# Performance work log

Measured on AMD Instinct MI355X. Metric: run time of the kernel, lower is better.

Reference implementation:

```python
import jax, jax.numpy as jnp
import numpy as np

D_MODEL = 1024
N_HEADS = 16
D_HEAD = D_MODEL // N_HEADS
GN_EPS = 1e-5


def setup_inputs() -> dict:
    key = jax.random.key(0)
    ks = jax.random.split(key, 5)
    B, T = 2, 2048
    s = 1.0 / np.sqrt(D_MODEL)
    x = jax.random.normal(ks[0], (B, T, D_MODEL), dtype=jnp.float32)
    W_q = jax.random.normal(ks[1], (D_MODEL, D_MODEL), dtype=jnp.float32) * s
    W_k = jax.random.normal(ks[2], (D_MODEL, D_MODEL), dtype=jnp.float32) * s
    W_v = jax.random.normal(ks[3], (D_MODEL, D_MODEL), dtype=jnp.float32) * s
    W_o = jax.random.normal(ks[4], (D_MODEL, D_MODEL), dtype=jnp.float32) * s
    gn_weight = jnp.ones((D_MODEL,), dtype=jnp.float32)
    gn_bias = jnp.zeros((D_MODEL,), dtype=jnp.float32)
    return {"x": x, "W_q": W_q, "W_k": W_k, "W_v": W_v, "W_o": W_o,
            "gn_weight": gn_weight, "gn_bias": gn_bias}


def reference(x, W_q, W_k, W_v, W_o, gn_weight, gn_bias):
    B, T, _ = x.shape
    H, Dh = N_HEADS, D_HEAD
    # Projections (nn.Linear: y = x @ W.T), split heads -> [B, T, H, Dh]
    q = (x @ W_q.T).reshape(B, T, H, Dh)
    k = (x @ W_k.T).reshape(B, T, H, Dh)
    v = (x @ W_v.T).reshape(B, T, H, Dh)

    # Per-head causal decay mask D_h[i, j] = gamma_h^(i-j) for i >= j else 0
    gammas = jnp.asarray([1.0 - 2.0 ** (-5.0 - i) for i in range(H)],
                         dtype=jnp.float32)  # [H]
    idx = jnp.arange(T, dtype=jnp.float32)
    diff = idx[:, None] - idx[None, :]  # [T, T]
    decay = jnp.where(diff >= 0,
                      gammas[:, None, None] ** jnp.maximum(diff, 0.0),
                      0.0)  # [H, T, T]

    scale = jnp.sqrt(jnp.asarray(Dh, dtype=x.dtype))
    qk = jnp.einsum('bthd,bshd->bhts', q, k)          # [B, H, T, T]
    attn = qk * decay[None] / scale
    y = jnp.einsum('bhts,bshd->bthd', attn, v)        # [B, T, H, Dh]

    # GroupNorm(n_heads groups) over channels-last-transposed layout:
    # torch applies it to [B, d_model, T]; each group = one head's Dh channels,
    # normalized over (Dh, T).
    yg = y.transpose(0, 2, 3, 1)                      # [B, H, Dh, T]
    mean = yg.mean(axis=(2, 3), keepdims=True)
    var = yg.var(axis=(2, 3), keepdims=True)
    yn = (yg - mean) / jnp.sqrt(var + GN_EPS)
    yn = yn * gn_weight.reshape(1, H, Dh, 1) + gn_bias.reshape(1, H, Dh, 1)
    y = yn.transpose(0, 3, 1, 2).reshape(B, T, H * Dh)  # [B, T, d_model]
    return y @ W_o.T
```

## Files before the change

kernel.cpp:

```cpp
#include <hip/hip_runtime.h>
#include <math.h>

#define TSEQ 2048
#define NB   2
#define DM   1024
#define NH   16
#define DH   64
#define GN_EPS 1e-5f

typedef short v8s __attribute__((ext_vector_type(8)));
typedef short v4s __attribute__((ext_vector_type(4)));
typedef float v4f __attribute__((ext_vector_type(4)));

__device__ __forceinline__ short f2bf(float f) {
    union { float f; unsigned u; } c; c.f = f;
    unsigned u = c.u;
    unsigned r = (u + 0x7fffu + ((u >> 16) & 1u)) >> 16;
    return (short)r;
}
__device__ __forceinline__ float bf2f(short s) {
    union { unsigned u; float f; } c; c.u = ((unsigned)(unsigned short)s) << 16;
    return c.f;
}

__device__ __forceinline__ unsigned cvtpk_bf16(float lo, float hi) {
    unsigned r;
    asm("v_cvt_pk_bf16_f32 %0, %1, %2" : "=v"(r) : "v"(lo), "v"(hi));
    return r;
}

__device__ __forceinline__ void gl_lds16(const void* g, void* l) {
    __builtin_amdgcn_global_load_lds(
        (const __attribute__((address_space(1))) void*)g,
        (__attribute__((address_space(3))) void*)l, 16, 0, 0);
}

__global__ __launch_bounds__(256) void cast_kernel(
    const float* __restrict__ x,
    const float* __restrict__ Wq, const float* __restrict__ Wk,
    const float* __restrict__ Wv, const float* __restrict__ Wo,
    short* __restrict__ xbf, short* __restrict__ wbf)
{
    const int NX = NB * TSEQ * DM;
    const int NW = DM * DM;
    const int total4 = (NX + 4 * NW) / 4;
    for (int i = blockIdx.x * 256 + threadIdx.x; i < total4;
         i += gridDim.x * 256) {
        int e = i * 4;
        const float* src; short* dst;
        if (e < NX) { src = x + e; dst = xbf + e; }
        else {
            int o = e - NX;
            int w = o >> 20;
            int r = o & (NW - 1);
            src = (w == 0 ? Wq : w == 1 ? Wk : w == 2 ? Wv : Wo) + r;
            dst = wbf + o;
        }
        v4f v = *(const v4f*)src;
        v4s s;
        #pragma unroll
        for (int j = 0; j < 4; ++j) s[j] = f2bf(v[j]);
        *(v4s*)dst = s;
    }
}

__global__ __launch_bounds__(256, 3) void gemm_qkv_mfma(
    const short* __restrict__ xbf, const short* __restrict__ wbf,
    short* __restrict__ Qb, short* __restrict__ Kb,
    short* __restrict__ Kt, short* __restrict__ Vt)
{
    const int z = blockIdx.z;
    const short* __restrict__ Bmat = wbf + (size_t)z * (DM * DM);
    const int n0 = blockIdx.x * 128, m0 = blockIdx.y * 128;
    const int t = threadIdx.x, l = t & 63, w = t >> 6;
    const int wr = (w >> 1) * 64, wc = (w & 1) * 64;
    const int lr = l & 15, g = l >> 4, lg4 = g * 4;

    __shared__ short As[128 * 64];
    __shared__ short Bs[128 * 64];

    v4f acc[4][4];
    #pragma unroll
    for (int i = 0; i < 4; ++i)
        #pragma unroll
        for (int j = 0; j < 4; ++j) acc[i][j] = (v4f){0.f, 0.f, 0.f, 0.f};

    const char* Agp = (const char*)(xbf  + (size_t)m0 * DM);
    const char* Bgp = (const char*)(Bmat + (size_t)n0 * DM);

    int soff[4], sdst[4];
    #pragma unroll
    for (int p = 0; p < 4; ++p) {
        int i = p * 256 + t;
        int row = i >> 3;
        int cp  = (i & 7) * 16;
        soff[p] = row * (DM * 2) + (cp ^ ((row & 7) << 4));
        sdst[p] = (p * 256 + (t & 192)) * 16;
    }
    const int swz = (lr & 7) << 4;

    for (int kt = 0; kt < DM / 64; ++kt) {
        const int kb = kt * 128;
        #pragma unroll
        for (int p = 0; p < 4; ++p) {
            gl_lds16(Agp + (size_t)soff[p] + kb, (char*)As + sdst[p]);
            gl_lds16(Bgp + (size_t)soff[p] + kb, (char*)Bs + sdst[p]);
        }
        asm volatile("s_waitcnt vmcnt(0)" ::: "memory");
        __syncthreads();

        v8s bfr[4][2];
        #pragma unroll
        for (int j = 0; j < 4; ++j) {
            int rowb = wc + j * 16 + lr;
            #pragma unroll
            for (int ks = 0; ks < 2; ++ks)
                bfr[j][ks] = *(const v8s*)((const char*)Bs + rowb * 128
                               + ((ks * 64 + g * 16) ^ swz));
        }
        #pragma unroll
        for (int i = 0; i < 4; ++i) {
            int rowa = wr + i * 16 + lr;
            v8s a0 = *(const v8s*)((const char*)As + rowa * 128 + ((g * 16) ^ swz));
            v8s a1 = *(const v8s*)((const char*)As + rowa * 128 + ((64 + g * 16) ^ swz));
            #pragma unroll
            for (int j = 0; j < 4; ++j) {
                acc[i][j] = __builtin_amdgcn_mfma_f32_16x16x32_bf16(
                    a0, bfr[j][0], acc[i][j], 0, 0, 0);
                acc[i][j] = __builtin_amdgcn_mfma_f32_16x16x32_bf16(
                    a1, bfr[j][1], acc[i][j], 0, 0, 0);
            }
        }
        __syncthreads();
    }

    if (z == 0) {
        float l2gj[4];
        #pragma unroll
        for (int j = 0; j < 4; ++j) {
            int hh = (n0 + wc + j * 16 + lr) >> 6;
            l2gj[j] = log2f(1.0f - exp2f(-5.0f - (float)hh));
        }
        #pragma unroll
        for (int i = 0; i < 4; ++i) {
            int row = m0 + wr + i * 16 + lg4;
            #pragma unroll
            for (int j = 0; j < 4; ++j) {
                int col = n0 + wc + j * 16 + lr;
                #pragma unroll
                for (int r = 0; r < 4; ++r) {
                    int tl = (row + r) & 63;
                    float fac = exp2f(fmaf(l2gj[j], (float)tl, -3.0f));
                    Qb[(size_t)(row + r) * DM + col] = f2bf(acc[i][j][r] * fac);
                }
            }
        }
    } else if (z == 1) {
        float l2gj[4];
        #pragma unroll
        for (int j = 0; j < 4; ++j) {
            int hh = (n0 + wc + j * 16 + lr) >> 6;
            l2gj[j] = -log2f(1.0f - exp2f(-5.0f - (float)hh));
        }
        #pragma unroll
        for (int i = 0; i < 4; ++i) {
            int row  = m0 + wr + i * 16 + lg4;
            int bidx = row >> 11, tb = row & (TSEQ - 1);
            #pragma unroll
            for (int j = 0; j < 4; ++j) {
                int col = n0 + wc + j * 16 + lr;
                v4s pk;
                #pragma unroll
                for (int r = 0; r < 4; ++r) {
                    int tl = (row + r) & 63;
                    float fac = exp2f(l2gj[j] * (float)tl);
                    short bv = f2bf(acc[i][j][r] * fac);
                    Kb[(size_t)(row + r) * DM + col] = bv;
                    pk[r] = bv;
                }
                *(v4s*)(Kt + ((size_t)bidx << 21) + ((size_t)col << 11) + tb) = pk;
            }
        }
    } else {
        #pragma unroll
        for (int i = 0; i < 4; ++i) {
            int row  = m0 + wr + i * 16 + lg4;
            int bidx = row >> 11, tb = row & (TSEQ - 1);
            #pragma unroll
            for (int j = 0; j < 4; ++j) {
                int col = n0 + wc + j * 16 + lr;
                v4s pk;
                #pragma unroll
                for (int r = 0; r < 4; ++r) pk[r] = f2bf(acc[i][j][r]);
                *(v4s*)(Vt + ((size_t)bidx << 21) + ((size_t)col << 11) + tb) = pk;
            }
        }
    }
}

__global__ __launch_bounds__(256, 2) void chunk_kv(
    const short* __restrict__ Kt, const short* __restrict__ Vt,
    short* __restrict__ At)
{
    const int bid = blockIdx.x;
    const int c = bid & 31, bh = bid >> 5;
    const int b = bh >> 4, h = bh & 15;
    const int tid = threadIdx.x, l = tid & 63, w = tid >> 6;
    const int lr = l & 15, g = l >> 4;

    const size_t rowbase = ((size_t)b * DM + h * 64);

    v8s kf[2], vf[4][2];
    {
        const short* kp = Kt + (rowbase + 16 * w + lr) * TSEQ + 64 * c;
        kf[0] = *(const v8s*)(kp + g * 8);
        kf[1] = *(const v8s*)(kp + 32 + g * 8);
    }
    #pragma unroll
    for (int j = 0; j < 4; ++j) {
        const short* vp = Vt + (rowbase + j * 16 + lr) * TSEQ + 64 * c;
        vf[j][0] = *(const v8s*)(vp + g * 8);
        vf[j][1] = *(const v8s*)(vp + 32 + g * 8);
    }

    v4f acc[4];
    #pragma unroll
    for (int j = 0; j < 4; ++j) acc[j] = (v4f){0.f, 0.f, 0.f, 0.f};

    #pragma unroll
    for (int j = 0; j < 4; ++j) {
        acc[j] = __builtin_amdgcn_mfma_f32_16x16x32_bf16(kf[0], vf[j][0], acc[j], 0, 0, 0);
        acc[j] = __builtin_amdgcn_mfma_f32_16x16x32_bf16(kf[1], vf[j][1], acc[j], 0, 0, 0);
    }

    short* Ab = At + (((size_t)bh * 32 + c) << 12);
    #pragma unroll
    for (int j = 0; j < 4; ++j) {
        v4s pk;
        #pragma unroll
        for (int r = 0; r < 4; ++r) pk[r] = f2bf(acc[j][r]);
        *(v4s*)(Ab + (j * 16 + lr) * 64 + 16 * w + g * 4) = pk;
    }
}

__global__ __launch_bounds__(256) void chunk_scan(
    const short* __restrict__ At, short* __restrict__ St)
{
    const int idx = blockIdx.x * 256 + threadIdx.x;
    const int bh = idx >> 12;
    const int h  = bh & 15;
    const float l2g = log2f(1.0f - exp2f(-5.0f - (float)h));
    const float g64 = exp2f(l2g * 64.0f);

    const size_t base = ((size_t)bh << 17) + (idx & 4095);
    float state = 0.0f;
    #pragma unroll
    for (int c = 1; c < 32; ++c) {
        float a = bf2f(At[base + ((size_t)(c - 1) << 12)]);
        state = g64 * (state + a);
        St[base + ((size_t)c << 12)] = f2bf(state);
    }
}

__global__ __launch_bounds__(256, 2) void chunk_out(
    const short* __restrict__ Qb, const short* __restrict__ Kb,
    const short* __restrict__ Vt, const short* __restrict__ St,
    short* __restrict__ Ybf, float* __restrict__ psums)
{
    const int bid = blockIdx.x;
    const int xcd = bid & 7, r8 = bid >> 3;
    const int bh  = xcd * 4 + (r8 >> 5);
    const int c   = r8 & 31;
    const int b = bh >> 4, h = bh & 15;
    const int tid = threadIdx.x, l = tid & 63, w = tid >> 6;
    const int lr = l & 15, g = l >> 4;

    __shared__ short strip[64 * 64];
    __shared__ float tr[64][68];
    __shared__ float red[8];

    const size_t rowQK = ((size_t)(b * TSEQ + 64 * c)) * DM + h * 64;

    v8s qf[4][2];
    #pragma unroll
    for (int j = 0; j < 4; ++j) {
        const short* qp = Qb + rowQK + (size_t)(j * 16 + lr) * DM;
        qf[j][0] = *(const v8s*)(qp + g * 8);
        qf[j][1] = *(const v8s*)(qp + 32 + g * 8);
    }
    v8s kf0, kf1;
    {
        const short* kp = Kb + rowQK + (size_t)(16 * w + lr) * DM;
        kf0 = *(const v8s*)(kp + g * 8);
        kf1 = *(const v8s*)(kp + 32 + g * 8);
    }
    v8s sf0 = {}, sf1 = {};
    if (c > 0) {
        const short* sp = St + (((size_t)bh * 32 + c) << 12) + (16 * w + lr) * 64;
        sf0 = *(const v8s*)(sp + g * 8);
        sf1 = *(const v8s*)(sp + 32 + g * 8);
    }
    v8s vf0, vf1;
    {
        const short* vp = Vt + ((size_t)(b * DM + h * 64) + 16 * w + lr) * TSEQ
                          + 64 * c;
        vf0 = *(const v8s*)(vp + g * 8);
        vf1 = *(const v8s*)(vp + 32 + g * 8);
    }

    v4f s[4];
    #pragma unroll
    for (int j = 0; j < 4; ++j) {
        v4f a = (v4f){0.f, 0.f, 0.f, 0.f};
        a = __builtin_amdgcn_mfma_f32_16x16x32_bf16(kf0, qf[j][0], a, 0, 0, 0);
        a = __builtin_amdgcn_mfma_f32_16x16x32_bf16(kf1, qf[j][1], a, 0, 0, 0);
        s[j] = a;
    }

    v4f y[4];
    #pragma unroll
    for (int j = 0; j < 4; ++j) y[j] = (v4f){0.f, 0.f, 0.f, 0.f};
    if (c > 0) {
        #pragma unroll
        for (int j = 0; j < 4; ++j) {
            y[j] = __builtin_amdgcn_mfma_f32_16x16x32_bf16(sf0, qf[j][0], y[j], 0, 0, 0);
            y[j] = __builtin_amdgcn_mfma_f32_16x16x32_bf16(sf1, qf[j][1], y[j], 0, 0, 0);
        }
    }

    #pragma unroll
    for (int j = 0; j < 4; ++j) {
        v4f vv = s[j];
        #pragma unroll
        for (int r = 0; r < 4; ++r)
            if ((j * 16 + lr) - (16 * w + g * 4 + r) < 0) vv[r] = 0.0f;
        unsigned u0 = cvtpk_bf16(vv[0], vv[1]);
        unsigned u1 = cvtpk_bf16(vv[2], vv[3]);
        int byte = ((j * 16 + lr) * 128 + 32 * w + g * 8) ^ ((lr & 7) << 4);
        *(unsigned long long*)((char*)strip + byte) =
            (unsigned long long)u0 | ((unsigned long long)u1 << 32);
    }
    __syncthreads();

    #pragma unroll
    for (int j = 0; j < 4; ++j) {
        int rb = (j * 16 + lr) * 128;
        int sw = (lr & 7) << 4;
        v8s sB0 = *(const v8s*)((char*)strip + ((rb + g * 16) ^ sw));
        v8s sB1 = *(const v8s*)((char*)strip + ((rb + 64 + g * 16) ^ sw));
        y[j] = __builtin_amdgcn_mfma_f32_16x16x32_bf16(vf0, sB0, y[j], 0, 0, 0);
        y[j] = __builtin_amdgcn_mfma_f32_16x16x32_bf16(vf1, sB1, y[j], 0, 0, 0);
    }

    float lsum = 0.f, lsq = 0.f;
    #pragma unroll
    for (int j = 0; j < 4; ++j)
        #pragma unroll
        for (int r = 0; r < 4; ++r) {
            float vy = y[j][r];
            lsum += vy; lsq += vy * vy;
        }
    #pragma unroll
    for (int m = 32; m; m >>= 1) {
        lsum += __shfl_xor(lsum, m, 64);
        lsq  += __shfl_xor(lsq,  m, 64);
    }
    if (l == 0) { red[w] = lsum; red[4 + w] = lsq; }

    #pragma unroll
    for (int j = 0; j < 4; ++j)
        #pragma unroll
        for (int r = 0; r < 4; ++r)
            tr[j * 16 + lr][16 * w + g * 4 + r] = y[j][r];
    __syncthreads();

    if (tid == 0) {
        float* ps = psums + ((size_t)bh * 32 + c) * 2;
        ps[0] = red[0] + red[1] + red[2] + red[3];
        ps[1] = red[4] + red[5] + red[6] + red[7];
    }

    #pragma unroll
    for (int u = 0; u < 4; ++u) {
        int row  = (tid >> 4) + u * 16;
        int col4 = (tid & 15) * 4;
        v4f val = *(const v4f*)&tr[row][col4];
        v4s pk;
        #pragma unroll
        for (int r = 0; r < 4; ++r) pk[r] = f2bf(val[r]);
        *(v4s*)&Ybf[(size_t)(b * TSEQ + 64 * c + row) * DM + h * 64 + col4] = pk;
    }
}

__global__ __launch_bounds__(256) void gn_finalize(
    const float* __restrict__ psums,
    const float* __restrict__ gnw, const float* __restrict__ gnb,
    float* __restrict__ scale, float* __restrict__ shift)
{
    int idx = blockIdx.x * 256 + threadIdx.x;
    if (idx >= NB * DM) return;
    int bb = idx >> 10;
    int ch = idx & (DM - 1);
    int hh = ch >> 6;
    int bh = bb * 16 + hh;

    float s = 0.f, q = 0.f;
    #pragma unroll
    for (int k = 0; k < 32; ++k) {
        s += psums[((size_t)bh * 32 + k) * 2];
        q += psums[((size_t)bh * 32 + k) * 2 + 1];
    }
    const float n = (float)(DH * TSEQ);
    float mean = s / n;
    float var  = q / n - mean * mean;
    float rstd = rsqrtf(var + GN_EPS);
    float sc = rstd * gnw[ch];
    scale[idx] = sc;
    shift[idx] = gnb[ch] - mean * sc;
}

__global__ __launch_bounds__(256) void wo_prep(
    const short* __restrict__ Wob, const float* __restrict__ scale,
    const float* __restrict__ shift,
    short* __restrict__ Wo2, float* __restrict__ bias)
{
    const int tid = threadIdx.x, l = tid & 63, w = tid >> 6;
    const int bn = blockIdx.x * 4 + w;
    const int b = bn >> 10, n = bn & 1023;
    const int k0 = l * 16;

    const short* wp = Wob + (size_t)n * DM + k0;
    v8s w0 = *(const v8s*)wp;
    v8s w1 = *(const v8s*)(wp + 8);
    const float* sc = scale + b * DM + k0;
    const float* sh = shift + b * DM + k0;

    v8s o0, o1;
    float bsum = 0.f;
    #pragma unroll
    for (int j = 0; j < 8; ++j) {
        float wf = bf2f(w0[j]);
        o0[j] = f2bf(wf * sc[j]);
        bsum = fmaf(sh[j], wf, bsum);
    }
    #pragma unroll
    for (int j = 0; j < 8; ++j) {
        float wf = bf2f(w1[j]);
        o1[j] = f2bf(wf * sc[8 + j]);
        bsum = fmaf(sh[8 + j], wf, bsum);
    }
    short* op = Wo2 + ((size_t)b * DM + n) * DM + k0;
    *(v8s*)op = o0;
    *(v8s*)(op + 8) = o1;

    #pragma unroll
    for (int m = 32; m; m >>= 1) bsum += __shfl_xor(bsum, m, 64);
    if (l == 0) bias[bn] = bsum;
}

__global__ __launch_bounds__(256, 3) void gemm_out_mfma(
    const short* __restrict__ Ybf, const short* __restrict__ Wo2,
    const float* __restrict__ bias, float* __restrict__ out)
{
    const int n0 = blockIdx.x * 128, m0 = blockIdx.y * 128;
    const int b = m0 >> 11;
    const int t = threadIdx.x, l = t & 63, w = t >> 6;
    const int wr = (w >> 1) * 64, wc = (w & 1) * 64;
    const int lr = l & 15, g = l >> 4;

    __shared__ short As[128 * 64];
    __shared__ short Bs[128 * 64];

    v4f acc[4][4];
    #pragma unroll
    for (int i = 0; i < 4; ++i)
        #pragma unroll
        for (int j = 0; j < 4; ++j) acc[i][j] = (v4f){0.f, 0.f, 0.f, 0.f};

    const char* Agp = (const char*)(Ybf + (size_t)m0 * DM);
    const char* Bgp = (const char*)(Wo2 + (size_t)b * DM * DM + (size_t)n0 * DM);

    int soff[4], sdst[4];
    #pragma unroll
    for (int p = 0; p < 4; ++p) {
        int i = p * 256 + t;
        int row = i >> 3;
        int cp  = (i & 7) * 16;
        soff[p] = row * (DM * 2) + (cp ^ ((row & 7) << 4));
        sdst[p] = (p * 256 + (t & 192)) * 16;
    }
    const int swz = (lr & 7) << 4;

    for (int kt = 0; kt < DM / 64; ++kt) {
        const int kb = kt * 128;
        #pragma unroll
        for (int p = 0; p < 4; ++p) {
            gl_lds16(Agp + (size_t)soff[p] + kb, (char*)As + sdst[p]);
            gl_lds16(Bgp + (size_t)soff[p] + kb, (char*)Bs + sdst[p]);
        }
        asm volatile("s_waitcnt vmcnt(0)" ::: "memory");
        __syncthreads();

        v8s bfr[4][2];
        #pragma unroll
        for (int j = 0; j < 4; ++j) {
            int rowb = wc + j * 16 + lr;
            #pragma unroll
            for (int ks = 0; ks < 2; ++ks)
                bfr[j][ks] = *(const v8s*)((const char*)Bs + rowb * 128
                               + ((ks * 64 + g * 16) ^ swz));
        }
        #pragma unroll
        for (int i = 0; i < 4; ++i) {
            int rowa = wr + i * 16 + lr;
            v8s a0 = *(const v8s*)((const char*)As + rowa * 128 + ((g * 16) ^ swz));
            v8s a1 = *(const v8s*)((const char*)As + rowa * 128 + ((64 + g * 16) ^ swz));
            #pragma unroll
            for (int j = 0; j < 4; ++j) {
                acc[i][j] = __builtin_amdgcn_mfma_f32_16x16x32_bf16(
                    a0, bfr[j][0], acc[i][j], 0, 0, 0);
                acc[i][j] = __builtin_amdgcn_mfma_f32_16x16x32_bf16(
                    a1, bfr[j][1], acc[i][j], 0, 0, 0);
            }
        }
        __syncthreads();
    }

    #pragma unroll
    for (int i = 0; i < 4; ++i) {
        int row = m0 + wr + i * 16 + g * 4;
        #pragma unroll
        for (int j = 0; j < 4; ++j) {
            int col = n0 + wc + j * 16 + lr;
            float bv = bias[b * DM + col];
            #pragma unroll
            for (int r = 0; r < 4; ++r)
                out[(size_t)(row + r) * DM + col] = acc[i][j][r] + bv;
        }
    }
}

extern "C" void kernel_launch(void* const* d_in, const int* in_sizes, int n_in,
                              void* d_out, int out_size, void* d_ws, size_t ws_size,
                              hipStream_t stream)
{
    const float* x   = (const float*)d_in[0];
    const float* Wq  = (const float*)d_in[1];
    const float* Wk  = (const float*)d_in[2];
    const float* Wv  = (const float*)d_in[3];
    const float* Wo  = (const float*)d_in[4];
    const float* gnw = (const float*)d_in[5];
    const float* gnb = (const float*)d_in[6];
    float* out = (float*)d_out;

    char* wsb = (char*)d_ws;
    size_t o = 0;
    short* Qb   = (short*)(wsb + o); o += (size_t)NB * TSEQ * DM * 2;
    short* Kb   = (short*)(wsb + o); o += (size_t)NB * TSEQ * DM * 2;
    short* Kt   = (short*)(wsb + o); o += (size_t)NB * TSEQ * DM * 2;
    short* Vt   = (short*)(wsb + o); o += (size_t)NB * TSEQ * DM * 2;
    short* xbf  = (short*)(wsb + o); o += (size_t)NB * TSEQ * DM * 2;
    short* wbf  = (short*)(wsb + o); o += (size_t)4 * DM * DM * 2;
    short* Ybf  = (short*)(wsb + o); o += (size_t)NB * TSEQ * DM * 2;
    short* St   = (short*)(wsb + o); o += (size_t)NB * TSEQ * DM * 2;
    short* Wo2  = (short*)(wsb + o); o += (size_t)NB * DM * DM * 2;
    float* psums = (float*)(wsb + o); o += (size_t)32 * 32 * 2 * 4;
    float* scale = (float*)(wsb + o); o += (size_t)NB * DM * 4;
    float* shift = (float*)(wsb + o); o += (size_t)NB * DM * 4;
    float* bias  = (float*)(wsb + o); o += (size_t)NB * DM * 4;
    if (ws_size < o) return;

    short* At = xbf;

    cast_kernel<<<2048, 256, 0, stream>>>(x, Wq, Wk, Wv, Wo, xbf, wbf);
    gemm_qkv_mfma<<<dim3(DM / 128, (NB * TSEQ) / 128, 3), 256, 0, stream>>>(
        xbf, wbf, Qb, Kb, Kt, Vt);
    chunk_kv<<<dim3(1024), 256, 0, stream>>>(Kt, Vt, At);
    chunk_scan<<<dim3(512), 256, 0, stream>>>(At, St);
    chunk_out<<<dim3(1024), 256, 0, stream>>>(Qb, Kb, Vt, St, Ybf, psums);
    gn_finalize<<<dim3((NB * DM + 255) / 256), 256, 0, stream>>>(
        psums, gnw, gnb, scale, shift);
    wo_prep<<<dim3(512), 256, 0, stream>>>(
        wbf + 3 * (size_t)DM * DM, scale, shift, Wo2, bias);
    gemm_out_mfma<<<dim3(DM / 128, (NB * TSEQ) / 128), 256, 0, stream>>>(
        Ybf, Wo2, bias, out);
}
```

Before: 95.69 us.

## Split QKV GEMM, swap MFMA operands for vectorized row stores, swizzle block order

Splits the fused QKV projection into a Q-only kernel and a K/V kernel. In the Q and output GEMMs the MFMA operands are swapped so that each lane holds four consecutive columns of one row, which allows packed 8-byte bf16 stores for Q and 16-byte float4 stores for the output in place of scalar strided stores. All GEMMs use a 1D grid with an XCD-style block swizzle to improve L2 locality. The cost is an extra kernel launch and two GEMMs that no longer share one launch.

```diff
diff --git a/kernel.cpp b/kernel.cpp
--- a/kernel.cpp
+++ b/kernel.cpp
@@ -64,17 +64,16 @@
     }
 }
 
-__global__ __launch_bounds__(256, 3) void gemm_qkv_mfma(
+__global__ __launch_bounds__(256, 3) void gemm_q_mfma(
     const short* __restrict__ xbf, const short* __restrict__ wbf,
-    short* __restrict__ Qb, short* __restrict__ Kb,
-    short* __restrict__ Kt, short* __restrict__ Vt)
-{
-    const int z = blockIdx.z;
-    const short* __restrict__ Bmat = wbf + (size_t)z * (DM * DM);
-    const int n0 = blockIdx.x * 128, m0 = blockIdx.y * 128;
+    short* __restrict__ Qb)
+{
+    const int bid = blockIdx.x;
+    const int swizb = (bid & 7) * 32 + (bid >> 3);
+    const int n0 = (swizb & 7) * 128, m0 = (swizb >> 3) * 128;
     const int t = threadIdx.x, l = t & 63, w = t >> 6;
     const int wr = (w >> 1) * 64, wc = (w & 1) * 64;
-    const int lr = l & 15, g = l >> 4, lg4 = g * 4;
+    const int lr = l & 15, g = l >> 4;
 
     __shared__ short As[128 * 64];
     __shared__ short Bs[128 * 64];
@@ -85,8 +84,8 @@
         #pragma unroll
         for (int j = 0; j < 4; ++j) acc[i][j] = (v4f){0.f, 0.f, 0.f, 0.f};
 
-    const char* Agp = (const char*)(xbf  + (size_t)m0 * DM);
-    const char* Bgp = (const char*)(Bmat + (size_t)n0 * DM);
+    const char* Agp = (const char*)(xbf + (size_t)m0 * DM);
+    const char* Bgp = (const char*)(wbf + (size_t)n0 * DM);
 
     int soff[4], sdst[4];
     #pragma unroll
@@ -126,6 +125,101 @@
             #pragma unroll
             for (int j = 0; j < 4; ++j) {
                 acc[i][j] = __builtin_amdgcn_mfma_f32_16x16x32_bf16(
+                    bfr[j][0], a0, acc[i][j], 0, 0, 0);
+                acc[i][j] = __builtin_amdgcn_mfma_f32_16x16x32_bf16(
+                    bfr[j][1], a1, acc[i][j], 0, 0, 0);
+            }
+        }
+        __syncthreads();
+    }
+
+    const int head = (n0 + wc) >> 6;
+    const float l2g = log2f(1.0f - exp2f(-5.0f - (float)head));
+    float fac[4];
+    #pragma unroll
+    for (int i = 0; i < 4; ++i) {
+        int tl = (m0 + wr + i * 16 + lr) & 63;
+        fac[i] = exp2f(fmaf(l2g, (float)tl, -3.0f));
+    }
+    #pragma unroll
+    for (int i = 0; i < 4; ++i) {
+        int mrow = m0 + wr + i * 16 + lr;
+        #pragma unroll
+        for (int j = 0; j < 4; ++j) {
+            int ncol = n0 + wc + j * 16 + g * 4;
+            v4s pk;
+            #pragma unroll
+            for (int r = 0; r < 4; ++r) pk[r] = f2bf(acc[i][j][r] * fac[i]);
+            *(v4s*)(Qb + (size_t)mrow * DM + ncol) = pk;
+        }
+    }
+}
+
+__global__ __launch_bounds__(256, 3) void gemm_kv_mfma(
+    const short* __restrict__ xbf, const short* __restrict__ wbf,
+    short* __restrict__ Kb, short* __restrict__ Kt, short* __restrict__ Vt)
+{
+    const int bid = blockIdx.x;
+    const int swizb = (bid & 7) * 64 + (bid >> 3);
+    const int z = swizb >> 8;
+    const int rem = swizb & 255;
+    const int n0 = (rem & 7) * 128, m0 = (rem >> 3) * 128;
+    const short* __restrict__ Bmat = wbf + (size_t)(z + 1) * (DM * DM);
+
+    const int t = threadIdx.x, l = t & 63, w = t >> 6;
+    const int wr = (w >> 1) * 64, wc = (w & 1) * 64;
+    const int lr = l & 15, g = l >> 4, lg4 = g * 4;
+
+    __shared__ short As[128 * 64];
+    __shared__ short Bs[128 * 64];
+
+    v4f acc[4][4];
+    #pragma unroll
+    for (int i = 0; i < 4; ++i)
+        #pragma unroll
+        for (int j = 0; j < 4; ++j) acc[i][j] = (v4f){0.f, 0.f, 0.f, 0.f};
+
+    const char* Agp = (const char*)(xbf  + (size_t)m0 * DM);
+    const char* Bgp = (const char*)(Bmat + (size_t)n0 * DM);
+
+    int soff[4], sdst[4];
+    #pragma unroll
+    for (int p = 0; p < 4; ++p) {
+        int i = p * 256 + t;
+        int row = i >> 3;
+        int cp  = (i & 7) * 16;
+        soff[p] = row * (DM * 2) + (cp ^ ((row & 7) << 4));
+        sdst[p] = (p * 256 + (t & 192)) * 16;
+    }
+    const int swz = (lr & 7) << 4;
+
+    for (int kt = 0; kt < DM / 64; ++kt) {
+        const int kb = kt * 128;
+        #pragma unroll
+        for (int p = 0; p < 4; ++p) {
+            gl_lds16(Agp + (size_t)soff[p] + kb, (char*)As + sdst[p]);
+            gl_lds16(Bgp + (size_t)soff[p] + kb, (char*)Bs + sdst[p]);
+        }
+        asm volatile("s_waitcnt vmcnt(0)" ::: "memory");
+        __syncthreads();
+
+        v8s bfr[4][2];
+        #pragma unroll
+        for (int j = 0; j < 4; ++j) {
+            int rowb = wc + j * 16 + lr;
+            #pragma unroll
+            for (int ks = 0; ks < 2; ++ks)
+                bfr[j][ks] = *(const v8s*)((const char*)Bs + rowb * 128
+                               + ((ks * 64 + g * 16) ^ swz));
+        }
+        #pragma unroll
+        for (int i = 0; i < 4; ++i) {
+            int rowa = wr + i * 16 + lr;
+            v8s a0 = *(const v8s*)((const char*)As + rowa * 128 + ((g * 16) ^ swz));
+            v8s a1 = *(const v8s*)((const char*)As + rowa * 128 + ((64 + g * 16) ^ swz));
+            #pragma unroll
+            for (int j = 0; j < 4; ++j) {
+                acc[i][j] = __builtin_amdgcn_mfma_f32_16x16x32_bf16(
                     a0, bfr[j][0], acc[i][j], 0, 0, 0);
                 acc[i][j] = __builtin_amdgcn_mfma_f32_16x16x32_bf16(
                     a1, bfr[j][1], acc[i][j], 0, 0, 0);
@@ -135,27 +229,6 @@
     }
 
     if (z == 0) {
-        float l2gj[4];
-        #pragma unroll
-        for (int j = 0; j < 4; ++j) {
-            int hh = (n0 + wc + j * 16 + lr) >> 6;
-            l2gj[j] = log2f(1.0f - exp2f(-5.0f - (float)hh));
-        }
-        #pragma unroll
-        for (int i = 0; i < 4; ++i) {
-            int row = m0 + wr + i * 16 + lg4;
-            #pragma unroll
-            for (int j = 0; j < 4; ++j) {
-                int col = n0 + wc + j * 16 + lr;
-                #pragma unroll
-                for (int r = 0; r < 4; ++r) {
-                    int tl = (row + r) & 63;
-                    float fac = exp2f(fmaf(l2gj[j], (float)tl, -3.0f));
-                    Qb[(size_t)(row + r) * DM + col] = f2bf(acc[i][j][r] * fac);
-                }
-            }
-        }
-    } else if (z == 1) {
         float l2gj[4];
         #pragma unroll
         for (int j = 0; j < 4; ++j) {
@@ -173,8 +246,8 @@
                 #pragma unroll
                 for (int r = 0; r < 4; ++r) {
                     int tl = (row + r) & 63;
-                    float fac = exp2f(l2gj[j] * (float)tl);
-                    short bv = f2bf(acc[i][j][r] * fac);
+                    float fc = exp2f(l2gj[j] * (float)tl);
+                    short bv = f2bf(acc[i][j][r] * fc);
                     Kb[(size_t)(row + r) * DM + col] = bv;
                     pk[r] = bv;
                 }
@@ -462,7 +535,9 @@
     const short* __restrict__ Ybf, const short* __restrict__ Wo2,
     const float* __restrict__ bias, float* __restrict__ out)
 {
-    const int n0 = blockIdx.x * 128, m0 = blockIdx.y * 128;
+    const int bid = blockIdx.x;
+    const int swizb = (bid & 7) * 32 + (bid >> 3);
+    const int n0 = (swizb & 7) * 128, m0 = (swizb >> 3) * 128;
     const int b = m0 >> 11;
     const int t = threadIdx.x, l = t & 63, w = t >> 6;
     const int wr = (w >> 1) * 64, wc = (w & 1) * 64;
@@ -518,9 +593,9 @@
             #pragma unroll
             for (int j = 0; j < 4; ++j) {
                 acc[i][j] = __builtin_amdgcn_mfma_f32_16x16x32_bf16(
-                    a0, bfr[j][0], acc[i][j], 0, 0, 0);
+                    bfr[j][0], a0, acc[i][j], 0, 0, 0);
                 acc[i][j] = __builtin_amdgcn_mfma_f32_16x16x32_bf16(
-                    a1, bfr[j][1], acc[i][j], 0, 0, 0);
+                    bfr[j][1], a1, acc[i][j], 0, 0, 0);
             }
         }
         __syncthreads();
@@ -528,14 +603,13 @@
 
     #pragma unroll
     for (int i = 0; i < 4; ++i) {
-        int row = m0 + wr + i * 16 + g * 4;
+        int mrow = m0 + wr + i * 16 + lr;
         #pragma unroll
         for (int j = 0; j < 4; ++j) {
-            int col = n0 + wc + j * 16 + lr;
-            float bv = bias[b * DM + col];
-            #pragma unroll
-            for (int r = 0; r < 4; ++r)
-                out[(size_t)(row + r) * DM + col] = acc[i][j][r] + bv;
+            int ncol = n0 + wc + j * 16 + g * 4;
+            v4f bv = *(const v4f*)&bias[b * DM + ncol];
+            v4f o = acc[i][j] + bv;
+            *(v4f*)&out[(size_t)mrow * DM + ncol] = o;
         }
     }
 }
@@ -573,8 +647,8 @@
     short* At = xbf;
 
     cast_kernel<<<2048, 256, 0, stream>>>(x, Wq, Wk, Wv, Wo, xbf, wbf);
-    gemm_qkv_mfma<<<dim3(DM / 128, (NB * TSEQ) / 128, 3), 256, 0, stream>>>(
-        xbf, wbf, Qb, Kb, Kt, Vt);
+    gemm_q_mfma<<<dim3(256), 256, 0, stream>>>(xbf, wbf, Qb);
+    gemm_kv_mfma<<<dim3(512), 256, 0, stream>>>(xbf, wbf, Kb, Kt, Vt);
     chunk_kv<<<dim3(1024), 256, 0, stream>>>(Kt, Vt, At);
     chunk_scan<<<dim3(512), 256, 0, stream>>>(At, St);
     chunk_out<<<dim3(1024), 256, 0, stream>>>(Qb, Kb, Vt, St, Ybf, psums);
@@ -582,6 +656,5 @@
         psums, gnw, gnb, scale, shift);
     wo_prep<<<dim3(512), 256, 0, stream>>>(
         wbf + 3 * (size_t)DM * DM, scale, shift, Wo2, bias);
-    gemm_out_mfma<<<dim3(DM / 128, (NB * TSEQ) / 128), 256, 0, stream>>>(
-        Ybf, Wo2, bias, out);
-}
+    gemm_out_mfma<<<dim3(256), 256, 0, stream>>>(Ybf, Wo2, bias, out);
+}
```

After: 108.8 us. +13.7%, slower.
